# Performance work log

Hardware: AMD Instinct MI355X
Metric: run time of the kernel (lower is better)

Reference implementation:

```python
import jax, jax.numpy as jnp
import numpy as np

N, IN_DIM, OUT_DIM = 8192, 256, 64
NEG_INF = -9e15
SLOPE = 0.2


def setup_inputs() -> dict:
    key = jax.random.key(0)
    k1, k2, k3, k4 = jax.random.split(key, 4)
    h = jax.random.normal(k1, (N, IN_DIM), dtype=jnp.float32)
    adj = jax.random.randint(k2, (N, N), 0, 2, dtype=jnp.int32)
    W = jax.random.normal(k3, (IN_DIM, OUT_DIM), dtype=jnp.float32) * (1.0 / np.sqrt(IN_DIM))
    a = jax.random.normal(k4, (2 * OUT_DIM,), dtype=jnp.float32) * (1.0 / np.sqrt(2 * OUT_DIM))
    return {"h": h, "adj": adj, "W": W, "a": a}


def reference(h, adj, W, a):
    # Wh: [N, F]
    Wh = h @ W
    F = Wh.shape[-1]
    # a([Wh_i ; Wh_j]) decomposes: score_ij = a_left.Wh_i + a_right.Wh_j
    f_i = Wh @ a[:F]          # [N]
    f_j = Wh @ a[F:]          # [N]
    e = f_i[:, None] + f_j[None, :]            # [N, N] broadcast sum
    e = jnp.where(e >= 0, e, SLOPE * e)         # leaky relu (0.2)
    e = jnp.where(adj > 0, e, jnp.float32(NEG_INF))
    alpha = jax.nn.softmax(e, axis=1)           # row softmax over neighbors j
    return alpha @ Wh                            # [N, F]
```

## Files before the change

kernel.cpp:

```cpp
#include <hip/hip_runtime.h>
#include <hip/hip_fp16.h>

#define NN 8192
#define KDIM 256
#define FDIM 64

typedef __attribute__((ext_vector_type(8))) _Float16 f16x8;
typedef __attribute__((ext_vector_type(4))) float f32x4;
typedef __attribute__((ext_vector_type(4))) int i32x4;

union H2U { __half2 h; unsigned u; };
union HU  { __half h; unsigned short u; };

__device__ __forceinline__ unsigned h2u(__half2 h) { H2U x; x.h = h; return x.u; }

__device__ __forceinline__ unsigned pkmul(unsigned a, unsigned b) {
    unsigned d; asm("v_pk_mul_f16 %0, %1, %2" : "=v"(d) : "v"(a), "v"(b)); return d;
}
__device__ __forceinline__ unsigned pkmax(unsigned a, unsigned b) {
    unsigned d; asm("v_pk_max_f16 %0, %1, %2" : "=v"(d) : "v"(a), "v"(b)); return d;
}

__device__ __forceinline__ float wred64(float v) {
    v += __shfl_xor(v, 1);
    v += __shfl_xor(v, 2);
    v += __shfl_xor(v, 4);
    v += __shfl_xor(v, 8);
    v += __shfl_xor(v, 16);
    v += __shfl_xor(v, 32);
    return v;
}

__global__ __launch_bounds__(256) void gat_phase1(
    const float* __restrict__ h, const float* __restrict__ W,
    const float* __restrict__ a, unsigned short* __restrict__ wfrag,
    float* __restrict__ fi, float* __restrict__ fj)
{
    __shared__ unsigned short wht_s[FDIM][20];
    const int tid = threadIdx.x;
    const int f  = tid & 63;
    const int rg = tid >> 6;
    const int i0 = blockIdx.x << 4;

    const float* __restrict__ h0 = h + (size_t)(i0 + rg * 4) * KDIM;
    const float* __restrict__ h1 = h0 + KDIM;
    const float* __restrict__ h2 = h0 + 2 * KDIM;
    const float* __restrict__ h3 = h0 + 3 * KDIM;

    float acc0 = 0.f, acc1 = 0.f, acc2 = 0.f, acc3 = 0.f;
    #pragma unroll 4
    for (int k4 = 0; k4 < KDIM / 4; ++k4) {
        const float4 r0 = *(const float4*)(h0 + k4 * 4);
        const float4 r1 = *(const float4*)(h1 + k4 * 4);
        const float4 r2 = *(const float4*)(h2 + k4 * 4);
        const float4 r3 = *(const float4*)(h3 + k4 * 4);
        const float w0 = W[(k4 * 4 + 0) * FDIM + f];
        const float w1 = W[(k4 * 4 + 1) * FDIM + f];
        const float w2 = W[(k4 * 4 + 2) * FDIM + f];
        const float w3 = W[(k4 * 4 + 3) * FDIM + f];
        acc0 += r0.x * w0 + r0.y * w1 + r0.z * w2 + r0.w * w3;
        acc1 += r1.x * w0 + r1.y * w1 + r1.z * w2 + r1.w * w3;
        acc2 += r2.x * w0 + r2.y * w1 + r2.z * w2 + r2.w * w3;
        acc3 += r3.x * w0 + r3.y * w1 + r3.z * w2 + r3.w * w3;
    }

    HU c0; c0.h = __float2half(acc0);
    HU c1; c1.h = __float2half(acc1);
    HU c2; c2.h = __float2half(acc2);
    HU c3; c3.h = __float2half(acc3);
    const int r0i = rg * 4;
    wht_s[f][r0i + 0] = c0.u;
    wht_s[f][r0i + 1] = c1.u;
    wht_s[f][r0i + 2] = c2.u;
    wht_s[f][r0i + 3] = c3.u;

    const float aL = a[f];
    const float aR = a[FDIM + f];
    float s;
    s = wred64(acc0 * aL); if (f == 0) fi[i0 + r0i + 0] = s;
    s = wred64(acc1 * aL); if (f == 0) fi[i0 + r0i + 1] = s;
    s = wred64(acc2 * aL); if (f == 0) fi[i0 + r0i + 2] = s;
    s = wred64(acc3 * aL); if (f == 0) fi[i0 + r0i + 3] = s;
    s = wred64(acc0 * aR); if (f == 0) fj[i0 + r0i + 0] = s;
    s = wred64(acc1 * aR); if (f == 0) fj[i0 + r0i + 1] = s;
    s = wred64(acc2 * aR); if (f == 0) fj[i0 + r0i + 2] = s;
    s = wred64(acc3 * aR); if (f == 0) fj[i0 + r0i + 3] = s;

    __syncthreads();
    if (tid < 128) {
        const int li2 = tid & 15;
        const int q2  = (tid >> 4) & 1;
        const int b   = tid >> 5;
        const int t   = i0 >> 5;
        const int hh  = (i0 >> 4) & 1;
        const int feat = b * 16 + li2;
        const ushort4 lo = *(const ushort4*)&wht_s[feat][q2 * 8];
        const ushort4 hi = *(const ushort4*)&wht_s[feat][q2 * 8 + 4];
        const int lg = (hh * 2 + q2) * 16 + li2;
        unsigned short* dst = wfrag + (size_t)t * 2048 + b * 512 + lg * 8;
        *(ushort4*)(dst)     = lo;
        *(ushort4*)(dst + 4) = hi;
    }
}

__global__ __launch_bounds__(512, 4) void gat_fused(
    const int* __restrict__ adj, const unsigned short* __restrict__ wfrag,
    const float* __restrict__ fi, const float* __restrict__ fjg,
    float* __restrict__ vpart, float* __restrict__ zpart)
{
    __shared__ unsigned mask_lds[16][129];
    __shared__ unsigned Ebuf[4096];
    __shared__ float zred[128];

    const int tid = threadIdx.x;
    const int w  = tid >> 6;
    const int l  = tid & 63;
    const int li = l & 15;
    const int q  = l >> 4;
    const int qo = q * 8;
    const int bid  = blockIdx.x;
    const int i0   = (bid >> 1) << 4;
    const int half = bid & 1;

    unsigned* E1p = Ebuf;
    unsigned* E2p = Ebuf + 2048;
    for (int t = tid; t < 2048; t += 512) {
        const float2 f2 = ((const float2*)fjg)[half * 2048 + t];
        E1p[t] = h2u(__floats2half2_rn(__expf(f2.x), __expf(f2.y)));
        E2p[t] = h2u(__floats2half2_rn(__expf(0.2f * f2.x), __expf(0.2f * f2.y)));
    }

    const int wsel = (l & 7) * 4;
    #pragma unroll
    for (int j = 0; j < 2; ++j) {
        const int r = 2 * w + j;
        const i32x4* __restrict__ rowp =
            (const i32x4*)(adj + (size_t)(i0 + r) * NN + half * (NN / 2));
        #pragma unroll 1
        for (int g = 0; g < 16; g += 8) {
            i32x4 v[8];
            #pragma unroll
            for (int k = 0; k < 8; ++k)
                v[k] = __builtin_nontemporal_load(&rowp[(g + k) * 64 + l]);
            #pragma unroll
            for (int k = 0; k < 8; ++k) {
                unsigned nib = (unsigned)(v[k][0] > 0) | ((unsigned)(v[k][1] > 0) << 1)
                             | ((unsigned)(v[k][2] > 0) << 2) | ((unsigned)(v[k][3] > 0) << 3);
                unsigned part = nib << wsel;
                part |= __shfl_xor(part, 1);
                part |= __shfl_xor(part, 2);
                part |= __shfl_xor(part, 4);
                if ((l & 7) == 0) mask_lds[r][(g + k) * 8 + (l >> 3)] = part;
            }
        }
    }

    const float fiv = fi[i0 + li];
    const unsigned e1i2 = h2u(__floats2half2_rn(__expf(fiv), __expf(fiv)));
    const unsigned e2i2 = h2u(__floats2half2_rn(__expf(0.2f * fiv), __expf(0.2f * fiv)));
    const unsigned short* __restrict__ wf = wfrag + (size_t)(half * 128) * 2048 + l * 8;

    __syncthreads();

    f32x4 acc0 = {0.f, 0.f, 0.f, 0.f};
    f32x4 acc1 = {0.f, 0.f, 0.f, 0.f};
    f32x4 acc2 = {0.f, 0.f, 0.f, 0.f};
    f32x4 acc3 = {0.f, 0.f, 0.f, 0.f};
    f32x4 accz = {0.f, 0.f, 0.f, 0.f};
    const f16x8 ones = { (_Float16)1.f, (_Float16)1.f, (_Float16)1.f, (_Float16)1.f,
                         (_Float16)1.f, (_Float16)1.f, (_Float16)1.f, (_Float16)1.f };

    #pragma unroll 4
    for (int s = 0; s < 16; ++s) {
        const int tw = w + 8 * s;
        const unsigned mword = mask_lds[li][tw];
        const unsigned mq8 = (mword >> qo) & 0xFFu;
        const int ep = tw * 16 + q * 4;
        const uint4 e1w = *(const uint4*)(E1p + ep);
        const uint4 e2w = *(const uint4*)(E2p + ep);
        const unsigned short* wt = wf + (size_t)tw * 2048;
        const f16x8 b0 = *(const f16x8*)(wt);
        const f16x8 b1 = *(const f16x8*)(wt + 512);
        const f16x8 b2 = *(const f16x8*)(wt + 1024);
        const f16x8 b3 = *(const f16x8*)(wt + 1536);

        const unsigned mm0 = ((mq8 &   1u) ? 0x0000FFFFu : 0u) | ((mq8 &   2u) ? 0xFFFF0000u : 0u);
        const unsigned mm1 = ((mq8 &   4u) ? 0x0000FFFFu : 0u) | ((mq8 &   8u) ? 0xFFFF0000u : 0u);
        const unsigned mm2 = ((mq8 &  16u) ? 0x0000FFFFu : 0u) | ((mq8 &  32u) ? 0xFFFF0000u : 0u);
        const unsigned mm3 = ((mq8 &  64u) ? 0x0000FFFFu : 0u) | ((mq8 & 128u) ? 0xFFFF0000u : 0u);

        union { unsigned u[4]; f16x8 v; } af;
        af.u[0] = pkmax(pkmul(e1i2, e1w.x), pkmul(e2i2, e2w.x)) & mm0;
        af.u[1] = pkmax(pkmul(e1i2, e1w.y), pkmul(e2i2, e2w.y)) & mm1;
        af.u[2] = pkmax(pkmul(e1i2, e1w.z), pkmul(e2i2, e2w.z)) & mm2;
        af.u[3] = pkmax(pkmul(e1i2, e1w.w), pkmul(e2i2, e2w.w)) & mm3;

        acc0 = __builtin_amdgcn_mfma_f32_16x16x32_f16(af.v, b0, acc0, 0, 0, 0);
        acc1 = __builtin_amdgcn_mfma_f32_16x16x32_f16(af.v, b1, acc1, 0, 0, 0);
        acc2 = __builtin_amdgcn_mfma_f32_16x16x32_f16(af.v, b2, acc2, 0, 0, 0);
        acc3 = __builtin_amdgcn_mfma_f32_16x16x32_f16(af.v, b3, acc3, 0, 0, 0);
        accz = __builtin_amdgcn_mfma_f32_16x16x32_f16(af.v, ones, accz, 0, 0, 0);
    }

    __syncthreads();
    float* red4 = (float*)Ebuf;
    if (li == 0) {
        #pragma unroll
        for (int r = 0; r < 4; ++r)
            zred[w * 16 + q * 4 + r] = accz[r];
    }
    if (w < 4) {
        #pragma unroll
        for (int r = 0; r < 4; ++r) {
            red4[(w * 16 + q * 4 + r) * 64 + 0 * 16 + li] = acc0[r];
            red4[(w * 16 + q * 4 + r) * 64 + 1 * 16 + li] = acc1[r];
            red4[(w * 16 + q * 4 + r) * 64 + 2 * 16 + li] = acc2[r];
            red4[(w * 16 + q * 4 + r) * 64 + 3 * 16 + li] = acc3[r];
        }
    }
    __syncthreads();
    if (w >= 4) {
        #pragma unroll
        for (int r = 0; r < 4; ++r) {
            red4[((w - 4) * 16 + q * 4 + r) * 64 + 0 * 16 + li] += acc0[r];
            red4[((w - 4) * 16 + q * 4 + r) * 64 + 1 * 16 + li] += acc1[r];
            red4[((w - 4) * 16 + q * 4 + r) * 64 + 2 * 16 + li] += acc2[r];
            red4[((w - 4) * 16 + q * 4 + r) * 64 + 3 * 16 + li] += acc3[r];
        }
    }
    __syncthreads();

    const int f  = tid & 63;
    const int ig = tid >> 6;
    #pragma unroll
    for (int cc = 0; cc < 2; ++cc) {
        const int i = cc * 8 + ig;
        const float v = (red4[(0 * 16 + i) * 64 + f] + red4[(1 * 16 + i) * 64 + f])
                      + (red4[(2 * 16 + i) * 64 + f] + red4[(3 * 16 + i) * 64 + f]);
        vpart[(size_t)(half * NN + i0 + i) * FDIM + f] = v;
        if (f == 0) {
            const float zz = ((zred[0 * 16 + i] + zred[1 * 16 + i]) + (zred[2 * 16 + i] + zred[3 * 16 + i]))
                           + ((zred[4 * 16 + i] + zred[5 * 16 + i]) + (zred[6 * 16 + i] + zred[7 * 16 + i]));
            zpart[half * NN + i0 + i] = zz;
        }
    }
}

__global__ __launch_bounds__(256) void gat_merge(
    const float* __restrict__ vpart, const float* __restrict__ zpart,
    float* __restrict__ out)
{
    const int g = blockIdx.x * 256 + threadIdx.x;
    const float4 a = ((const float4*)vpart)[g];
    const float4 b = ((const float4*)vpart)[g + NN * FDIM / 4];
    const int row = g >> 4;
    const float z = zpart[row] + zpart[row + NN];
    float4 o;
    o.x = (a.x + b.x) / z;
    o.y = (a.y + b.y) / z;
    o.z = (a.z + b.z) / z;
    o.w = (a.w + b.w) / z;
    ((float4*)out)[g] = o;
}

extern "C" void kernel_launch(void* const* d_in, const int* in_sizes, int n_in,
                              void* d_out, int out_size, void* d_ws, size_t ws_size,
                              hipStream_t stream) {
    const float* h   = (const float*)d_in[0];
    const int*   adj = (const int*)d_in[1];
    const float* W   = (const float*)d_in[2];
    const float* a   = (const float*)d_in[3];
    float* out = (float*)d_out;

    unsigned short* wfrag = (unsigned short*)d_ws;
    float* fi = (float*)((char*)d_ws + (size_t)NN * FDIM * 2);
    float* fj = fi + NN;
    float* vpart = (float*)((char*)d_ws + (2u << 20));
    float* zpart = (float*)((char*)d_ws + (6u << 20));

    gat_phase1<<<NN / 16, 256, 0, stream>>>(h, W, a, wfrag, fi, fj);
    gat_fused<<<NN / 8, 512, 0, stream>>>(adj, wfrag, fi, fj, vpart, zpart);
    gat_merge<<<NN * FDIM / 1024, 256, 0, stream>>>(vpart, zpart, out);
}
```

Before: 93.55 us.

## Stream adjacency mask in chunks, double-buffered and overlapped with MFMA compute

Previously each block loaded its whole 16x4096 adjacency slab into an LDS bitmask before any MFMA work started. Now the adjacency is processed in 8 chunks. Loads for chunk c+2 are issued and chunk c+1 is ballot-packed into the alternate LDS buffer while chunk c is consumed by the MFMAs. The goal is to hide the HBM read latency of the int32 adjacency behind compute. In exchange it adds a __syncthreads per chunk, holds more live registers for the prefetched vectors, and changes which tiles each wave handles.

```diff
diff --git a/kernel.cpp b/kernel.cpp
--- a/kernel.cpp
+++ b/kernel.cpp
@@ -108,7 +108,7 @@
     const float* __restrict__ fi, const float* __restrict__ fjg,
     float* __restrict__ vpart, float* __restrict__ zpart)
 {
-    __shared__ unsigned mask_lds[16][129];
+    __shared__ unsigned mask_lds[2][16][17];
     __shared__ unsigned Ebuf[4096];
     __shared__ float zred[128];
 
@@ -130,36 +130,47 @@
         E2p[t] = h2u(__floats2half2_rn(__expf(0.2f * f2.x), __expf(0.2f * f2.y)));
     }
 
-    const int wsel = (l & 7) * 4;
-    #pragma unroll
-    for (int j = 0; j < 2; ++j) {
-        const int r = 2 * w + j;
-        const i32x4* __restrict__ rowp =
-            (const i32x4*)(adj + (size_t)(i0 + r) * NN + half * (NN / 2));
-        #pragma unroll 1
-        for (int g = 0; g < 16; g += 8) {
-            i32x4 v[8];
-            #pragma unroll
-            for (int k = 0; k < 8; ++k)
-                v[k] = __builtin_nontemporal_load(&rowp[(g + k) * 64 + l]);
-            #pragma unroll
-            for (int k = 0; k < 8; ++k) {
-                unsigned nib = (unsigned)(v[k][0] > 0) | ((unsigned)(v[k][1] > 0) << 1)
-                             | ((unsigned)(v[k][2] > 0) << 2) | ((unsigned)(v[k][3] > 0) << 3);
-                unsigned part = nib << wsel;
-                part |= __shfl_xor(part, 1);
-                part |= __shfl_xor(part, 2);
-                part |= __shfl_xor(part, 4);
-                if ((l & 7) == 0) mask_lds[r][(g + k) * 8 + (l >> 3)] = part;
-            }
-        }
-    }
-
     const float fiv = fi[i0 + li];
     const unsigned e1i2 = h2u(__floats2half2_rn(__expf(fiv), __expf(fiv)));
     const unsigned e2i2 = h2u(__floats2half2_rn(__expf(0.2f * fiv), __expf(0.2f * fiv)));
     const unsigned short* __restrict__ wf = wfrag + (size_t)(half * 128) * 2048 + l * 8;
-
+    const i32x4* __restrict__ rowp0 =
+        (const i32x4*)(adj + (size_t)(i0 + 2 * w) * NN + half * (NN / 2));
+    const i32x4* __restrict__ rowp1 =
+        (const i32x4*)(adj + (size_t)(i0 + 2 * w + 1) * NN + half * (NN / 2));
+    const int wsel = (l & 7) * 4;
+
+    i32x4 vA0, vA1, vA2, vA3, vB0, vB1, vB2, vB3;
+
+    #define LDADJ(c, d0, d1, d2, d3)                                          \
+        do { const int _b = (c) * 128;                                        \
+             d0 = __builtin_nontemporal_load(&rowp0[_b + l]);                 \
+             d1 = __builtin_nontemporal_load(&rowp0[_b + 64 + l]);            \
+             d2 = __builtin_nontemporal_load(&rowp1[_b + l]);                 \
+             d3 = __builtin_nontemporal_load(&rowp1[_b + 64 + l]); } while (0)
+
+    #define BALLOT_WR(cc, d0, d1, d2, d3)                                     \
+        do { const int _buf = (cc) & 1;                                       \
+             const i32x4 _v[4] = {d0, d1, d2, d3};                            \
+             _Pragma("unroll")                                                \
+             for (int _j = 0; _j < 2; ++_j)                                   \
+             for (int _k = 0; _k < 2; ++_k) {                                 \
+                 const i32x4 _x = _v[_j * 2 + _k];                            \
+                 unsigned _nib = (unsigned)(_x[0] > 0)                        \
+                               | ((unsigned)(_x[1] > 0) << 1)                 \
+                               | ((unsigned)(_x[2] > 0) << 2)                 \
+                               | ((unsigned)(_x[3] > 0) << 3);                \
+                 unsigned _p = _nib << wsel;                                  \
+                 _p |= __shfl_xor(_p, 1);                                     \
+                 _p |= __shfl_xor(_p, 2);                                     \
+                 _p |= __shfl_xor(_p, 4);                                     \
+                 if ((l & 7) == 0)                                            \
+                     mask_lds[_buf][2 * w + _j][8 * _k + (l >> 3)] = _p;      \
+             } } while (0)
+
+    LDADJ(0, vA0, vA1, vA2, vA3);
+    BALLOT_WR(0, vA0, vA1, vA2, vA3);
+    LDADJ(1, vA0, vA1, vA2, vA3);
     __syncthreads();
 
     f32x4 acc0 = {0.f, 0.f, 0.f, 0.f};
@@ -170,39 +181,50 @@
     const f16x8 ones = { (_Float16)1.f, (_Float16)1.f, (_Float16)1.f, (_Float16)1.f,
                          (_Float16)1.f, (_Float16)1.f, (_Float16)1.f, (_Float16)1.f };
 
-    #pragma unroll 4
-    for (int s = 0; s < 16; ++s) {
-        const int tw = w + 8 * s;
-        const unsigned mword = mask_lds[li][tw];
-        const unsigned mq8 = (mword >> qo) & 0xFFu;
-        const int ep = tw * 16 + q * 4;
-        const uint4 e1w = *(const uint4*)(E1p + ep);
-        const uint4 e2w = *(const uint4*)(E2p + ep);
-        const unsigned short* wt = wf + (size_t)tw * 2048;
-        const f16x8 b0 = *(const f16x8*)(wt);
-        const f16x8 b1 = *(const f16x8*)(wt + 512);
-        const f16x8 b2 = *(const f16x8*)(wt + 1024);
-        const f16x8 b3 = *(const f16x8*)(wt + 1536);
-
-        const unsigned mm0 = ((mq8 &   1u) ? 0x0000FFFFu : 0u) | ((mq8 &   2u) ? 0xFFFF0000u : 0u);
-        const unsigned mm1 = ((mq8 &   4u) ? 0x0000FFFFu : 0u) | ((mq8 &   8u) ? 0xFFFF0000u : 0u);
-        const unsigned mm2 = ((mq8 &  16u) ? 0x0000FFFFu : 0u) | ((mq8 &  32u) ? 0xFFFF0000u : 0u);
-        const unsigned mm3 = ((mq8 &  64u) ? 0x0000FFFFu : 0u) | ((mq8 & 128u) ? 0xFFFF0000u : 0u);
-
-        union { unsigned u[4]; f16x8 v; } af;
-        af.u[0] = pkmax(pkmul(e1i2, e1w.x), pkmul(e2i2, e2w.x)) & mm0;
-        af.u[1] = pkmax(pkmul(e1i2, e1w.y), pkmul(e2i2, e2w.y)) & mm1;
-        af.u[2] = pkmax(pkmul(e1i2, e1w.z), pkmul(e2i2, e2w.z)) & mm2;
-        af.u[3] = pkmax(pkmul(e1i2, e1w.w), pkmul(e2i2, e2w.w)) & mm3;
-
-        acc0 = __builtin_amdgcn_mfma_f32_16x16x32_f16(af.v, b0, acc0, 0, 0, 0);
-        acc1 = __builtin_amdgcn_mfma_f32_16x16x32_f16(af.v, b1, acc1, 0, 0, 0);
-        acc2 = __builtin_amdgcn_mfma_f32_16x16x32_f16(af.v, b2, acc2, 0, 0, 0);
-        acc3 = __builtin_amdgcn_mfma_f32_16x16x32_f16(af.v, b3, acc3, 0, 0, 0);
-        accz = __builtin_amdgcn_mfma_f32_16x16x32_f16(af.v, ones, accz, 0, 0, 0);
-    }
-
-    __syncthreads();
+    #pragma unroll 2
+    for (int c = 0; c < 8; ++c) {
+        const int buf = c & 1;
+        const int twl0 = 2 * w;
+        const int gtw0 = c * 16 + twl0;
+        const unsigned short* wt0 = wf + (size_t)gtw0 * 2048;
+        const f16x8 B00 = *(const f16x8*)(wt0);
+        const f16x8 B01 = *(const f16x8*)(wt0 + 512);
+        const f16x8 B02 = *(const f16x8*)(wt0 + 1024);
+        const f16x8 B03 = *(const f16x8*)(wt0 + 1536);
+        const f16x8 B10 = *(const f16x8*)(wt0 + 2048);
+        const f16x8 B11 = *(const f16x8*)(wt0 + 2560);
+        const f16x8 B12 = *(const f16x8*)(wt0 + 3072);
+        const f16x8 B13 = *(const f16x8*)(wt0 + 3584);
+        if (c + 2 < 8) LDADJ(c + 2, vB0, vB1, vB2, vB3);
+        #pragma unroll
+        for (int t2 = 0; t2 < 2; ++t2) {
+            const int twl = twl0 + t2;
+            const int gtw = gtw0 + t2;
+            const unsigned mword = mask_lds[buf][li][twl];
+            const unsigned mq8 = (mword >> qo) & 0xFFu;
+            const int ep = gtw * 16 + q * 4;
+            const uint4 e1w = *(const uint4*)(E1p + ep);
+            const uint4 e2w = *(const uint4*)(E2p + ep);
+            const unsigned mm0 = ((mq8 &   1u) ? 0x0000FFFFu : 0u) | ((mq8 &   2u) ? 0xFFFF0000u : 0u);
+            const unsigned mm1 = ((mq8 &   4u) ? 0x0000FFFFu : 0u) | ((mq8 &   8u) ? 0xFFFF0000u : 0u);
+            const unsigned mm2 = ((mq8 &  16u) ? 0x0000FFFFu : 0u) | ((mq8 &  32u) ? 0xFFFF0000u : 0u);
+            const unsigned mm3 = ((mq8 &  64u) ? 0x0000FFFFu : 0u) | ((mq8 & 128u) ? 0xFFFF0000u : 0u);
+            union { unsigned u[4]; f16x8 v; } af;
+            af.u[0] = pkmax(pkmul(e1i2, e1w.x), pkmul(e2i2, e2w.x)) & mm0;
+            af.u[1] = pkmax(pkmul(e1i2, e1w.y), pkmul(e2i2, e2w.y)) & mm1;
+            af.u[2] = pkmax(pkmul(e1i2, e1w.z), pkmul(e2i2, e2w.z)) & mm2;
+            af.u[3] = pkmax(pkmul(e1i2, e1w.w), pkmul(e2i2, e2w.w)) & mm3;
+            acc0 = __builtin_amdgcn_mfma_f32_16x16x32_f16(af.v, t2 ? B10 : B00, acc0, 0, 0, 0);
+            acc1 = __builtin_amdgcn_mfma_f32_16x16x32_f16(af.v, t2 ? B11 : B01, acc1, 0, 0, 0);
+            acc2 = __builtin_amdgcn_mfma_f32_16x16x32_f16(af.v, t2 ? B12 : B02, acc2, 0, 0, 0);
+            acc3 = __builtin_amdgcn_mfma_f32_16x16x32_f16(af.v, t2 ? B13 : B03, acc3, 0, 0, 0);
+            accz = __builtin_amdgcn_mfma_f32_16x16x32_f16(af.v, ones, accz, 0, 0, 0);
+        }
+        if (c + 1 < 8) BALLOT_WR(c + 1, vA0, vA1, vA2, vA3);
+        vA0 = vB0; vA1 = vB1; vA2 = vB2; vA3 = vB3;
+        __syncthreads();
+    }
+
     float* red4 = (float*)Ebuf;
     if (li == 0) {
         #pragma unroll
@@ -233,8 +255,8 @@
     const int f  = tid & 63;
     const int ig = tid >> 6;
     #pragma unroll
-    for (int cc = 0; cc < 2; ++cc) {
-        const int i = cc * 8 + ig;
+    for (int cc2 = 0; cc2 < 2; ++cc2) {
+        const int i = cc2 * 8 + ig;
         const float v = (red4[(0 * 16 + i) * 64 + f] + red4[(1 * 16 + i) * 64 + f])
                       + (red4[(2 * 16 + i) * 64 + f] + red4[(3 * 16 + i) * 64 + f]);
         vpart[(size_t)(half * NN + i0 + i) * FDIM + f] = v;
```

Measured after the change: 101.3 us. 8.3% more time.

## Split adjacency columns into eight segments with smaller blocks and wider merge

Applied to the files above, without the earlier changes.

The fused kernel now splits each 16-row tile's columns into eight 1024-column segments instead of two halves, using 256-thread blocks instead of 512. The launch grows from 1024 to 4096 blocks, and each block uses less shared memory, which should improve occupancy and latency hiding on the adj stream. The merge kernel now sums eight partial V/Z sets instead of two. In exchange, the partial workspace grows to about 16 MB of extra traffic, and each block repeats more exp and mask-setup overhead.

```diff
diff --git a/kernel.cpp b/kernel.cpp
--- a/kernel.cpp
+++ b/kernel.cpp
@@ -4,6 +4,8 @@
 #define NN 8192
 #define KDIM 256
 #define FDIM 64
+#define CBLK 1024
+#define NSEG (NN / CBLK)
 
 typedef __attribute__((ext_vector_type(8))) _Float16 f16x8;
 typedef __attribute__((ext_vector_type(4))) float f32x4;
@@ -103,14 +105,15 @@
     }
 }
 
-__global__ __launch_bounds__(512, 4) void gat_fused(
+__global__ __launch_bounds__(256, 4) void gat_fused(
     const int* __restrict__ adj, const unsigned short* __restrict__ wfrag,
     const float* __restrict__ fi, const float* __restrict__ fjg,
     float* __restrict__ vpart, float* __restrict__ zpart)
 {
-    __shared__ unsigned mask_lds[16][129];
-    __shared__ unsigned Ebuf[4096];
-    __shared__ float zred[128];
+    __shared__ unsigned mask_lds[16][33];
+    __shared__ unsigned Ebuf[1024];
+    __shared__ float red[2 * 16 * 64];
+    __shared__ float zred[4][16];
 
     const int tid = threadIdx.x;
     const int w  = tid >> 6;
@@ -118,47 +121,49 @@
     const int li = l & 15;
     const int q  = l >> 4;
     const int qo = q * 8;
-    const int bid  = blockIdx.x;
-    const int i0   = (bid >> 1) << 4;
-    const int half = bid & 1;
+    const int bid = blockIdx.x;
+    const int seg = bid & (NSEG - 1);
+    const int i0  = (bid / NSEG) << 4;
 
     unsigned* E1p = Ebuf;
-    unsigned* E2p = Ebuf + 2048;
-    for (int t = tid; t < 2048; t += 512) {
-        const float2 f2 = ((const float2*)fjg)[half * 2048 + t];
+    unsigned* E2p = Ebuf + 512;
+    for (int t = tid; t < 512; t += 256) {
+        const float2 f2 = ((const float2*)fjg)[seg * 512 + t];
         E1p[t] = h2u(__floats2half2_rn(__expf(f2.x), __expf(f2.y)));
         E2p[t] = h2u(__floats2half2_rn(__expf(0.2f * f2.x), __expf(0.2f * f2.y)));
     }
 
     const int wsel = (l & 7) * 4;
     #pragma unroll
-    for (int j = 0; j < 2; ++j) {
-        const int r = 2 * w + j;
-        const i32x4* __restrict__ rowp =
-            (const i32x4*)(adj + (size_t)(i0 + r) * NN + half * (NN / 2));
-        #pragma unroll 1
-        for (int g = 0; g < 16; g += 8) {
-            i32x4 v[8];
-            #pragma unroll
-            for (int k = 0; k < 8; ++k)
-                v[k] = __builtin_nontemporal_load(&rowp[(g + k) * 64 + l]);
-            #pragma unroll
-            for (int k = 0; k < 8; ++k) {
-                unsigned nib = (unsigned)(v[k][0] > 0) | ((unsigned)(v[k][1] > 0) << 1)
-                             | ((unsigned)(v[k][2] > 0) << 2) | ((unsigned)(v[k][3] > 0) << 3);
-                unsigned part = nib << wsel;
-                part |= __shfl_xor(part, 1);
-                part |= __shfl_xor(part, 2);
-                part |= __shfl_xor(part, 4);
-                if ((l & 7) == 0) mask_lds[r][(g + k) * 8 + (l >> 3)] = part;
-            }
+    for (int rp = 0; rp < 2; ++rp) {
+        const int r0 = 4 * w + 2 * rp;
+        const i32x4* __restrict__ p0 =
+            (const i32x4*)(adj + (size_t)(i0 + r0) * NN + seg * CBLK);
+        const i32x4* __restrict__ p1 = p0 + (NN / 4);
+        i32x4 v[8];
+        #pragma unroll
+        for (int k = 0; k < 4; ++k) v[k]     = __builtin_nontemporal_load(&p0[k * 64 + l]);
+        #pragma unroll
+        for (int k = 0; k < 4; ++k) v[4 + k] = __builtin_nontemporal_load(&p1[k * 64 + l]);
+        #pragma unroll
+        for (int k = 0; k < 8; ++k) {
+            const i32x4 x = v[k];
+            unsigned nib = (unsigned)(x[0] > 0) | ((unsigned)(x[1] > 0) << 1)
+                         | ((unsigned)(x[2] > 0) << 2) | ((unsigned)(x[3] > 0) << 3);
+            unsigned p = nib << wsel;
+            p |= __shfl_xor(p, 1);
+            p |= __shfl_xor(p, 2);
+            p |= __shfl_xor(p, 4);
+            const int rr = r0 + (k >> 2);
+            if ((l & 7) == 0) mask_lds[rr][(k & 3) * 8 + (l >> 3)] = p;
         }
     }
 
     const float fiv = fi[i0 + li];
     const unsigned e1i2 = h2u(__floats2half2_rn(__expf(fiv), __expf(fiv)));
     const unsigned e2i2 = h2u(__floats2half2_rn(__expf(0.2f * fiv), __expf(0.2f * fiv)));
-    const unsigned short* __restrict__ wf = wfrag + (size_t)(half * 128) * 2048 + l * 8;
+    const unsigned short* __restrict__ wf =
+        wfrag + (size_t)(seg * 32) * 2048 + l * 8;
 
     __syncthreads();
 
@@ -171,8 +176,8 @@
                          (_Float16)1.f, (_Float16)1.f, (_Float16)1.f, (_Float16)1.f };
 
     #pragma unroll 4
-    for (int s = 0; s < 16; ++s) {
-        const int tw = w + 8 * s;
+    for (int s = 0; s < 8; ++s) {
+        const int tw = w + 4 * s;
         const unsigned mword = mask_lds[li][tw];
         const unsigned mq8 = (mword >> qo) & 0xFFu;
         const int ep = tw * 16 + q * 4;
@@ -202,30 +207,28 @@
         accz = __builtin_amdgcn_mfma_f32_16x16x32_f16(af.v, ones, accz, 0, 0, 0);
     }
 
-    __syncthreads();
-    float* red4 = (float*)Ebuf;
     if (li == 0) {
         #pragma unroll
         for (int r = 0; r < 4; ++r)
-            zred[w * 16 + q * 4 + r] = accz[r];
-    }
-    if (w < 4) {
+            zred[w][q * 4 + r] = accz[r];
+    }
+    if (w < 2) {
         #pragma unroll
         for (int r = 0; r < 4; ++r) {
-            red4[(w * 16 + q * 4 + r) * 64 + 0 * 16 + li] = acc0[r];
-            red4[(w * 16 + q * 4 + r) * 64 + 1 * 16 + li] = acc1[r];
-            red4[(w * 16 + q * 4 + r) * 64 + 2 * 16 + li] = acc2[r];
-            red4[(w * 16 + q * 4 + r) * 64 + 3 * 16 + li] = acc3[r];
-        }
-    }
-    __syncthreads();
-    if (w >= 4) {
+            red[(w * 16 + q * 4 + r) * 64 + 0 * 16 + li] = acc0[r];
+            red[(w * 16 + q * 4 + r) * 64 + 1 * 16 + li] = acc1[r];
+            red[(w * 16 + q * 4 + r) * 64 + 2 * 16 + li] = acc2[r];
+            red[(w * 16 + q * 4 + r) * 64 + 3 * 16 + li] = acc3[r];
+        }
+    }
+    __syncthreads();
+    if (w >= 2) {
         #pragma unroll
         for (int r = 0; r < 4; ++r) {
-            red4[((w - 4) * 16 + q * 4 + r) * 64 + 0 * 16 + li] += acc0[r];
-            red4[((w - 4) * 16 + q * 4 + r) * 64 + 1 * 16 + li] += acc1[r];
-            red4[((w - 4) * 16 + q * 4 + r) * 64 + 2 * 16 + li] += acc2[r];
-            red4[((w - 4) * 16 + q * 4 + r) * 64 + 3 * 16 + li] += acc3[r];
+            red[((w - 2) * 16 + q * 4 + r) * 64 + 0 * 16 + li] += acc0[r];
+            red[((w - 2) * 16 + q * 4 + r) * 64 + 1 * 16 + li] += acc1[r];
+            red[((w - 2) * 16 + q * 4 + r) * 64 + 2 * 16 + li] += acc2[r];
+            red[((w - 2) * 16 + q * 4 + r) * 64 + 3 * 16 + li] += acc3[r];
         }
     }
     __syncthreads();
@@ -233,15 +236,13 @@
     const int f  = tid & 63;
     const int ig = tid >> 6;
     #pragma unroll
-    for (int cc = 0; cc < 2; ++cc) {
-        const int i = cc * 8 + ig;
-        const float v = (red4[(0 * 16 + i) * 64 + f] + red4[(1 * 16 + i) * 64 + f])
-                      + (red4[(2 * 16 + i) * 64 + f] + red4[(3 * 16 + i) * 64 + f]);
-        vpart[(size_t)(half * NN + i0 + i) * FDIM + f] = v;
+    for (int cc = 0; cc < 4; ++cc) {
+        const int i = cc * 4 + ig;
+        const float v = red[(0 * 16 + i) * 64 + f] + red[(1 * 16 + i) * 64 + f];
+        vpart[(size_t)(seg * NN + i0 + i) * FDIM + f] = v;
         if (f == 0) {
-            const float zz = ((zred[0 * 16 + i] + zred[1 * 16 + i]) + (zred[2 * 16 + i] + zred[3 * 16 + i]))
-                           + ((zred[4 * 16 + i] + zred[5 * 16 + i]) + (zred[6 * 16 + i] + zred[7 * 16 + i]));
-            zpart[half * NN + i0 + i] = zz;
+            const float zz = (zred[0][i] + zred[1][i]) + (zred[2][i] + zred[3][i]);
+            zpart[seg * NN + i0 + i] = zz;
         }
     }
 }
@@ -251,15 +252,17 @@
     float* __restrict__ out)
 {
     const int g = blockIdx.x * 256 + threadIdx.x;
-    const float4 a = ((const float4*)vpart)[g];
-    const float4 b = ((const float4*)vpart)[g + NN * FDIM / 4];
     const int row = g >> 4;
-    const float z = zpart[row] + zpart[row + NN];
+    float4 v = ((const float4*)vpart)[g];
+    float z = zpart[row];
+    #pragma unroll
+    for (int k = 1; k < NSEG; ++k) {
+        const float4 b = ((const float4*)vpart)[g + (size_t)k * NN * (FDIM / 4)];
+        v.x += b.x; v.y += b.y; v.z += b.z; v.w += b.w;
+        z += zpart[row + k * NN];
+    }
     float4 o;
-    o.x = (a.x + b.x) / z;
-    o.y = (a.y + b.y) / z;
-    o.z = (a.z + b.z) / z;
-    o.w = (a.w + b.w) / z;
+    o.x = v.x / z; o.y = v.y / z; o.z = v.z / z; o.w = v.w / z;
     ((float4*)out)[g] = o;
 }
 
@@ -276,9 +279,9 @@
     float* fi = (float*)((char*)d_ws + (size_t)NN * FDIM * 2);
     float* fj = fi + NN;
     float* vpart = (float*)((char*)d_ws + (2u << 20));
-    float* zpart = (float*)((char*)d_ws + (6u << 20));
+    float* zpart = (float*)((char*)d_ws + (18u << 20));
 
     gat_phase1<<<NN / 16, 256, 0, stream>>>(h, W, a, wfrag, fi, fj);
-    gat_fused<<<NN / 8, 512, 0, stream>>>(adj, wfrag, fi, fj, vpart, zpart);
+    gat_fused<<<(NN / 16) * NSEG, 256, 0, stream>>>(adj, wfrag, fi, fj, vpart, zpart);
     gat_merge<<<NN * FDIM / 1024, 256, 0, stream>>>(vpart, zpart, out);
 }
```

Result: no change. 92.75 us (-0.8%).

## Process full rows per block and fuse normalization, removing the merge kernel

Applied to the files above, without the earlier changes.

Each block now covers all 8192 columns for its 16 rows instead of splitting the columns in half across two blocks. The softmax normalization is done in-kernel, so the partial-sum buffers and the separate merge launch go away. The adjacency loads also switch from nontemporal to regular loads. In exchange the grid halves to 512 blocks, each running twice as long, and LDS use doubles (~50KB), which may reduce occupancy and leave CUs underused.

```diff
diff --git a/kernel.cpp b/kernel.cpp
--- a/kernel.cpp
+++ b/kernel.cpp
@@ -106,11 +106,11 @@
 __global__ __launch_bounds__(512, 4) void gat_fused(
     const int* __restrict__ adj, const unsigned short* __restrict__ wfrag,
     const float* __restrict__ fi, const float* __restrict__ fjg,
-    float* __restrict__ vpart, float* __restrict__ zpart)
+    float* __restrict__ out)
 {
-    __shared__ unsigned mask_lds[16][129];
-    __shared__ unsigned Ebuf[4096];
-    __shared__ float zred[128];
+    __shared__ unsigned mask_lds[16][257];
+    __shared__ unsigned Ebuf[8192];
+    __shared__ float zred[8][16];
 
     const int tid = threadIdx.x;
     const int w  = tid >> 6;
@@ -118,39 +118,37 @@
     const int li = l & 15;
     const int q  = l >> 4;
     const int qo = q * 8;
-    const int bid  = blockIdx.x;
-    const int i0   = (bid >> 1) << 4;
-    const int half = bid & 1;
+    const int i0 = blockIdx.x << 4;
 
     unsigned* E1p = Ebuf;
-    unsigned* E2p = Ebuf + 2048;
-    for (int t = tid; t < 2048; t += 512) {
-        const float2 f2 = ((const float2*)fjg)[half * 2048 + t];
+    unsigned* E2p = Ebuf + 4096;
+    for (int t = tid; t < 4096; t += 512) {
+        const float2 f2 = ((const float2*)fjg)[t];
         E1p[t] = h2u(__floats2half2_rn(__expf(f2.x), __expf(f2.y)));
         E2p[t] = h2u(__floats2half2_rn(__expf(0.2f * f2.x), __expf(0.2f * f2.y)));
     }
 
     const int wsel = (l & 7) * 4;
     #pragma unroll
-    for (int j = 0; j < 2; ++j) {
-        const int r = 2 * w + j;
-        const i32x4* __restrict__ rowp =
-            (const i32x4*)(adj + (size_t)(i0 + r) * NN + half * (NN / 2));
+    for (int rr = 0; rr < 2; ++rr) {
+        const int row = 2 * w + rr;
+        const i32x4* __restrict__ row4 = (const i32x4*)(adj + (size_t)(i0 + row) * NN);
         #pragma unroll 1
-        for (int g = 0; g < 16; g += 8) {
+        for (int base = 0; base < 32; base += 8) {
             i32x4 v[8];
             #pragma unroll
             for (int k = 0; k < 8; ++k)
-                v[k] = __builtin_nontemporal_load(&rowp[(g + k) * 64 + l]);
+                v[k] = row4[(base + k) * 64 + l];
             #pragma unroll
             for (int k = 0; k < 8; ++k) {
-                unsigned nib = (unsigned)(v[k][0] > 0) | ((unsigned)(v[k][1] > 0) << 1)
-                             | ((unsigned)(v[k][2] > 0) << 2) | ((unsigned)(v[k][3] > 0) << 3);
-                unsigned part = nib << wsel;
-                part |= __shfl_xor(part, 1);
-                part |= __shfl_xor(part, 2);
-                part |= __shfl_xor(part, 4);
-                if ((l & 7) == 0) mask_lds[r][(g + k) * 8 + (l >> 3)] = part;
+                const i32x4 x = v[k];
+                unsigned nib = (unsigned)(x[0] > 0) | ((unsigned)(x[1] > 0) << 1)
+                             | ((unsigned)(x[2] > 0) << 2) | ((unsigned)(x[3] > 0) << 3);
+                unsigned p = nib << wsel;
+                p |= __shfl_xor(p, 1);
+                p |= __shfl_xor(p, 2);
+                p |= __shfl_xor(p, 4);
+                if ((l & 7) == 0) mask_lds[row][(base + k) * 8 + (l >> 3)] = p;
             }
         }
     }
@@ -158,7 +156,7 @@
     const float fiv = fi[i0 + li];
     const unsigned e1i2 = h2u(__floats2half2_rn(__expf(fiv), __expf(fiv)));
     const unsigned e2i2 = h2u(__floats2half2_rn(__expf(0.2f * fiv), __expf(0.2f * fiv)));
-    const unsigned short* __restrict__ wf = wfrag + (size_t)(half * 128) * 2048 + l * 8;
+    const unsigned short* __restrict__ wf = wfrag + l * 8;
 
     __syncthreads();
 
@@ -171,7 +169,7 @@
                          (_Float16)1.f, (_Float16)1.f, (_Float16)1.f, (_Float16)1.f };
 
     #pragma unroll 4
-    for (int s = 0; s < 16; ++s) {
+    for (int s = 0; s < 32; ++s) {
         const int tw = w + 8 * s;
         const unsigned mword = mask_lds[li][tw];
         const unsigned mq8 = (mword >> qo) & 0xFFu;
@@ -207,7 +205,7 @@
     if (li == 0) {
         #pragma unroll
         for (int r = 0; r < 4; ++r)
-            zred[w * 16 + q * 4 + r] = accz[r];
+            zred[w][q * 4 + r] = accz[r];
     }
     if (w < 4) {
         #pragma unroll
@@ -237,30 +235,10 @@
         const int i = cc * 8 + ig;
         const float v = (red4[(0 * 16 + i) * 64 + f] + red4[(1 * 16 + i) * 64 + f])
                       + (red4[(2 * 16 + i) * 64 + f] + red4[(3 * 16 + i) * 64 + f]);
-        vpart[(size_t)(half * NN + i0 + i) * FDIM + f] = v;
-        if (f == 0) {
-            const float zz = ((zred[0 * 16 + i] + zred[1 * 16 + i]) + (zred[2 * 16 + i] + zred[3 * 16 + i]))
-                           + ((zred[4 * 16 + i] + zred[5 * 16 + i]) + (zred[6 * 16 + i] + zred[7 * 16 + i]));
-            zpart[half * NN + i0 + i] = zz;
-        }
-    }
-}
-
-__global__ __launch_bounds__(256) void gat_merge(
-    const float* __restrict__ vpart, const float* __restrict__ zpart,
-    float* __restrict__ out)
-{
-    const int g = blockIdx.x * 256 + threadIdx.x;
-    const float4 a = ((const float4*)vpart)[g];
-    const float4 b = ((const float4*)vpart)[g + NN * FDIM / 4];
-    const int row = g >> 4;
-    const float z = zpart[row] + zpart[row + NN];
-    float4 o;
-    o.x = (a.x + b.x) / z;
-    o.y = (a.y + b.y) / z;
-    o.z = (a.z + b.z) / z;
-    o.w = (a.w + b.w) / z;
-    ((float4*)out)[g] = o;
+        const float z = ((zred[0][i] + zred[1][i]) + (zred[2][i] + zred[3][i]))
+                      + ((zred[4][i] + zred[5][i]) + (zred[6][i] + zred[7][i]));
+        out[(size_t)(i0 + i) * FDIM + f] = v / z;
+    }
 }
 
 extern "C" void kernel_launch(void* const* d_in, const int* in_sizes, int n_in,
@@ -275,10 +253,7 @@
     unsigned short* wfrag = (unsigned short*)d_ws;
     float* fi = (float*)((char*)d_ws + (size_t)NN * FDIM * 2);
     float* fj = fi + NN;
-    float* vpart = (float*)((char*)d_ws + (2u << 20));
-    float* zpart = (float*)((char*)d_ws + (6u << 20));
 
     gat_phase1<<<NN / 16, 256, 0, stream>>>(h, W, a, wfrag, fi, fj);
-    gat_fused<<<NN / 8, 512, 0, stream>>>(adj, wfrag, fi, fj, vpart, zpart);
-    gat_merge<<<NN * FDIM / 1024, 256, 0, stream>>>(vpart, zpart, out);
-}
+    gat_fused<<<NN / 16, 512, 0, stream>>>(adj, wfrag, fi, fj, out);
+}
```

New measurement: 104.1 us. +11.3%, slower.
